# Kernel tuning notes

Measured on AMD Instinct MI355X. Metric: run time of the kernel, lower is better.

Reference implementation:

```python
import jax, jax.numpy as jnp
import numpy as np
import math

N = 50000        # nodes
DEG = 16         # regular out-degree -> E = N*DEG edges, grouped by source node
B = 64           # graphs in batch
F = 128          # num_node_features
H = 128          # nhid == enhid
RATIO = 0.5      # edge_ratio
NUM_CONVS = 3
E = N * DEG


def setup_inputs() -> dict:
    key = jax.random.key(0)
    ks = jax.random.split(key, 18)
    s = 0.05
    x = jax.random.normal(ks[0], (N, F), jnp.float32)
    edge_src = jnp.repeat(jnp.arange(N, dtype=jnp.int32), DEG)          # sorted by src
    edge_dst = jax.random.randint(ks[1], (E,), 0, N, jnp.int32)
    batch = ((jnp.arange(N) * B) // N).astype(jnp.int32)                 # sorted graph ids
    edge_attr = jnp.ones((E, 1), jnp.float32)                            # edge_attr=None branch
    inp = {"x": x, "edge_attr": edge_attr, "edge_src": edge_src,
           "edge_dst": edge_dst, "batch": batch}
    # GCNConv weights: [F->H, H->H, H->H]
    inp["W_gcn0"] = jax.random.normal(ks[2], (F, H), jnp.float32) * s
    inp["b_gcn0"] = jnp.zeros((H,), jnp.float32)
    inp["W_gcn1"] = jax.random.normal(ks[3], (H, H), jnp.float32) * s
    inp["b_gcn1"] = jnp.zeros((H,), jnp.float32)
    inp["W_gcn2"] = jax.random.normal(ks[4], (H, H), jnp.float32) * s
    inp["b_gcn2"] = jnp.zeros((H,), jnp.float32)
    # EGNN edge convs: [1->H, H->H]
    inp["W_eg0"] = jax.random.normal(ks[5], (1, H), jnp.float32) * s
    inp["b_eg0"] = jnp.zeros((H,), jnp.float32)
    inp["W_eg1"] = jax.random.normal(ks[6], (H, H), jnp.float32) * s
    inp["b_eg1"] = jnp.zeros((H,), jnp.float32)
    # score convs: [H->1, H->1]
    inp["W_sc0"] = jax.random.normal(ks[7], (H, 1), jnp.float32) * s
    inp["b_sc0"] = jnp.zeros((1,), jnp.float32)
    inp["W_sc1"] = jax.random.normal(ks[8], (H, 1), jnp.float32) * s
    inp["b_sc1"] = jnp.zeros((1,), jnp.float32)
    return inp


def _gcn(x, src, dst, ew, W, b):
    # PyG GCNConv: add self-loops (weight 1), symmetric deg normalization, aggregate at dst.
    n = x.shape[0]
    loop = jnp.arange(n, dtype=src.dtype)
    src2 = jnp.concatenate([src, loop])
    dst2 = jnp.concatenate([dst, loop])
    ew2 = jnp.concatenate([ew, jnp.ones((n,), ew.dtype)])
    deg = jax.ops.segment_sum(ew2, dst2, n)
    dinv = jnp.where(deg > 0, jax.lax.rsqrt(jnp.maximum(deg, 1e-12)), 0.0)
    norm = dinv[src2] * dinv[dst2] * ew2                                  # [E+n]
    msg = (x @ W)[src2] * norm[:, None]                                    # gather + scale
    return jax.ops.segment_sum(msg, dst2, n) + b                           # scatter-add


def _egnn(e, src, W, b):
    # Edge conv: scatter edge features to their source node, gather back, linear map.
    agg = jax.ops.segment_sum(e, src, N)
    return agg[src] @ W + b


def _pool(h, batch):
    gmax = jax.ops.segment_max(h, batch, B)
    gsum = jax.ops.segment_sum(h, batch, B)
    cnt = jax.ops.segment_sum(jnp.ones((h.shape[0],), h.dtype), batch, B)
    gmean = gsum / cnt[:, None]
    return jnp.concatenate([gmax, gmean, gsum], axis=1)                    # [B, 3H]


def reference(x, edge_attr, edge_src, edge_dst, batch,
              W_gcn0, b_gcn0, W_gcn1, b_gcn1, W_gcn2, b_gcn2,
              W_eg0, b_eg0, W_eg1, b_eg1, W_sc0, b_sc0, W_sc1, b_sc1):
    gW = [W_gcn0, W_gcn1, W_gcn2]
    gb = [b_gcn0, b_gcn1, b_gcn2]
    eW = [W_eg0, W_eg1]
    eb = [b_eg0, b_eg1]
    sW = [W_sc0, W_sc1]
    sb = [b_sc0, b_sc1]
    src, dst = edge_src, edge_dst
    deg = DEG
    ew = jnp.ones((src.shape[0],), jnp.float32)
    h = x
    ea = edge_attr
    xs = jnp.zeros((B, 3 * H), jnp.float32)
    for i in range(NUM_CONVS):
        h = jax.nn.relu(_gcn(h, src, dst, ew, gW[i], gb[i]))
        if i < NUM_CONVS - 1:
            ea = jax.nn.relu(_egnn(ea, src, eW[i], eb[i]))
            score = jnp.tanh(_egnn(ea, src, sW[i], sb[i])[:, 0])           # [E_cur]
            k = math.ceil(RATIO * deg)                                      # per-src-node top-k
            vals, idx = jax.lax.top_k(score.reshape(N, deg), k)             # [N,k]
            dst = jnp.take_along_axis(dst.reshape(N, deg), idx, axis=1).reshape(-1)
            flat = (jnp.arange(N)[:, None] * deg + idx).reshape(-1)
            ea = ea[flat]
            src = jnp.repeat(jnp.arange(N, dtype=src.dtype), k)
            ew = jnp.clip(vals.reshape(-1), 0.0, 1.0)
            deg = k
        xs = xs + _pool(h, batch)
    return xs
```

## Files before the change

### kernel.cpp

```cpp
#include <hip/hip_runtime.h>
#include <math.h>

#define NNODES 50000
#define DEGREE 16
#define NGRAPH 64
#define CAP 64
#define LDA 136
#define NXCD 8
#define XRANGE (NNODES / NXCD)
#define NTILE 782
#define ACHUNK 784
#define BCAP 192

typedef unsigned short u16;
typedef unsigned int u32;
typedef unsigned long long u64;
using short8 = __attribute__((ext_vector_type(8))) short;
using f32x4  = __attribute__((ext_vector_type(4))) float;
using fv4    = __attribute__((ext_vector_type(4))) float;
using u16x4  = __attribute__((ext_vector_type(4))) unsigned short;

__device__ __forceinline__ u16 f2bf(float f) {
  union { float f; u32 u; } v; v.f = f;
  u32 u = v.u;
  return (u16)((u + 0x7FFFu + ((u >> 16) & 1u)) >> 16);
}
__device__ __forceinline__ float2 bf2x2(u32 u) {
  union { u32 u; float f; } lo, hi;
  lo.u = (u & 0xFFFFu) << 16; hi.u = u & 0xFFFF0000u;
  return make_float2(lo.f, hi.f);
}
__device__ __forceinline__ u32 pack2(float x, float y) {
  return (u32)f2bf(x) | ((u32)f2bf(y) << 16);
}
__device__ __forceinline__ int lowerb(const int* b, int n, int v) {
  int lo = 0, hi = n;
  while (lo < hi) { int m = (lo + hi) >> 1; if (b[m] < v) lo = m + 1; else hi = m; }
  return lo;
}

__global__ __launch_bounds__(256) void k_init(
    const float* __restrict__ eattr, const float* __restrict__ x,
    const float* __restrict__ weg, const float* __restrict__ beg,
    const float* __restrict__ wsc, const float* __restrict__ bsc,
    const float* __restrict__ W0, const float* __restrict__ W1,
    const float* __restrict__ W2, const float* __restrict__ W3,
    float* __restrict__ ew1, float* __restrict__ agg0,
    u16* __restrict__ xb, u16* __restrict__ Wt,
    const int* __restrict__ edst, int* __restrict__ cnt,
    int* __restrict__ slots, int2* __restrict__ stag, int* __restrict__ scnt) {
  __shared__ int2 lbuf[NXCD * BCAP];
  __shared__ int lcnt[NXCD];
  int b = blockIdx.x, t = threadIdx.x;
  if (b < 6250) {
    int i = b * 256 + t;
    fv4 v = __builtin_nontemporal_load(&reinterpret_cast<const fv4*>(x)[i]);
    u16x4 o = {f2bf(v.x), f2bf(v.y), f2bf(v.z), f2bf(v.w)};
    reinterpret_cast<u16x4*>(xb)[i] = o;
    if (i < NNODES) {
      const fv4* p = reinterpret_cast<const fv4*>(eattr + (size_t)i * DEGREE);
      float s = 0.f;
#pragma unroll
      for (int j = 0; j < 4; ++j) {
        fv4 w = __builtin_nontemporal_load(&p[j]);
        s += w.x + w.y + w.z + w.w;
      }
      agg0[i] = s;
      float sc = 0.f;
      for (int k = 0; k < 128; ++k) {
        float e = fmaxf(fmaf(s, weg[k], beg[k]), 0.f);
        sc = fmaf(e, wsc[k], sc);
      }
      float v1 = tanhf(fmaf(16.f, sc, bsc[0]));
      ew1[i] = fminf(fmaxf(v1, 0.f), 1.f);
    }
  } else if (b < 6506) {
    int idx = (b - 6250) * 256 + t;
    int which = idx >> 14, r = idx & 16383;
    int k = r >> 7, n = r & 127;
    const float* W = which == 0 ? W0 : which == 1 ? W1 : which == 2 ? W2 : W3;
    Wt[which * 16384 + n * 128 + k] = f2bf(W[k * 128 + n]);
  } else {
    int b2 = b - 6506;
    if (t < NXCD) lcnt[t] = 0;
    __syncthreads();
    int e0 = b2 * ACHUNK;
    for (int k = 0; k < ACHUNK; k += 256) {
      int idx = k + t;
      int e = e0 + idx;
      if (idx < ACHUNK && e < NNODES * DEGREE) {
        int d = edst[e];
        u32 r = (u32)d / (u32)XRANGE;
        int pos = atomicAdd(&lcnt[r], 1);
        if (pos < BCAP) {
          lbuf[r * BCAP + pos] = make_int2(e, d);
        } else {
          int gp = atomicAdd(&cnt[d], 1);
          if (gp < CAP) slots[(size_t)d * CAP + gp] = e;
        }
      }
    }
    __syncthreads();
    for (int idx = t; idx < NXCD * BCAP; idx += 256) {
      int r = idx / BCAP, i = idx - r * BCAP;
      if (i < min(lcnt[r], BCAP))
        stag[((size_t)r * 1024 + b2) * BCAP + i] = lbuf[idx];
    }
    if (t < NXCD) scnt[t * 1024 + b2] = min(lcnt[t], BCAP);
  }
}

__global__ __launch_bounds__(256) void k_fillB(
    const int2* __restrict__ stag, const int* __restrict__ scnt,
    int* __restrict__ cnt, int* __restrict__ slots) {
  int kk = blockIdx.x;
  int r = kk & (NXCD - 1), sub = kk >> 3;
  for (int q = 0; q < 8; ++q) {
    int sb = sub * 8 + q;
    int c = scnt[r * 1024 + sb];
    const int2* src = &stag[((size_t)r * 1024 + sb) * BCAP];
    for (int i = threadIdx.x; i < c; i += 256) {
      int2 v = src[i];
      int pos = atomicAdd(&cnt[v.y], 1);
      if (pos < CAP) slots[(size_t)v.y * CAP + pos] = v.x;
    }
  }
}

__global__ __launch_bounds__(256) void k_gemmF(
    int nGemm, const u16* __restrict__ A, const u16* __restrict__ WtA,
    u16* __restrict__ outA,
    int nEg, const float* __restrict__ agg0, const float* __restrict__ weg,
    const float* __restrict__ beg, const u16* __restrict__ WtE,
    const float* __restrict__ beE, const float* __restrict__ wsc1,
    const float* __restrict__ bs1, float* __restrict__ ewOut) {
  __shared__ u16 Bs[128 * LDA];
  __shared__ u16 As[64 * LDA];
  int b = blockIdx.x, t = threadIdx.x;
  int eg = (b >= nGemm);
  const u16* Wsrc = eg ? WtE : WtA;
  for (int i = t; i < 2048; i += 256) {
    int r = i >> 4, c = (i & 15) << 3;
    *reinterpret_cast<uint4*>(&Bs[r * LDA + c]) =
        *reinterpret_cast<const uint4*>(&Wsrc[r * 128 + c]);
  }
  int m0 = (eg ? (b - nGemm) : b) * 64;
  if (eg) {
    for (int idx = t; idx < 64 * 128; idx += 256) {
      int r = idx >> 7, k = idx & 127;
      int row = m0 + r;
      float a = (row < NNODES) ? agg0[row] : 0.f;
      float v = 8.f * fmaxf(fmaf(a, weg[k], beg[k]), 0.f);
      As[r * LDA + k] = f2bf(v);
    }
  } else {
    for (int i = t; i < 1024; i += 256) {
      int r = i >> 4, c = (i & 15) << 3;
      int row = m0 + r;
      uint4 v = make_uint4(0u, 0u, 0u, 0u);
      if (row < NNODES) v = *reinterpret_cast<const uint4*>(&A[(size_t)row * 128 + c]);
      *reinterpret_cast<uint4*>(&As[r * LDA + c]) = v;
    }
  }
  __syncthreads();
  int wave = t >> 6, lane = t & 63;
  int lm = lane & 15, quad = lane >> 4;
  f32x4 z = {0.f, 0.f, 0.f, 0.f};
  f32x4 acc[8];
#pragma unroll
  for (int n = 0; n < 8; ++n) acc[n] = z;
  const u16* arow = &As[(wave * 16 + lm) * LDA + quad * 8];
#pragma unroll
  for (int kc = 0; kc < 4; ++kc) {
    short8 af = *reinterpret_cast<const short8*>(arow + kc * 32);
#pragma unroll
    for (int n = 0; n < 8; ++n) {
      short8 bf = *reinterpret_cast<const short8*>(
          &Bs[(n * 16 + lm) * LDA + kc * 32 + quad * 8]);
      acc[n] = __builtin_amdgcn_mfma_f32_16x16x32_bf16(af, bf, acc[n], 0, 0, 0);
    }
  }
  if (!eg) {
#pragma unroll
    for (int n = 0; n < 8; ++n) {
      int col = n * 16 + lm;
#pragma unroll
      for (int r = 0; r < 4; ++r) {
        int row = m0 + wave * 16 + quad * 4 + r;
        if (row < NNODES) outA[(size_t)row * 128 + col] = f2bf(acc[n][r]);
      }
    }
  } else {
    float s0 = 0.f, s1 = 0.f, s2 = 0.f, s3 = 0.f;
#pragma unroll
    for (int n = 0; n < 8; ++n) {
      int col = n * 16 + lm;
      float bb = beE[col], wv = wsc1[col];
      s0 = fmaf(fmaxf(acc[n][0] + bb, 0.f), wv, s0);
      s1 = fmaf(fmaxf(acc[n][1] + bb, 0.f), wv, s1);
      s2 = fmaf(fmaxf(acc[n][2] + bb, 0.f), wv, s2);
      s3 = fmaf(fmaxf(acc[n][3] + bb, 0.f), wv, s3);
    }
#pragma unroll
    for (int m = 8; m >= 1; m >>= 1) {
      s0 += __shfl_xor(s0, m, 64);
      s1 += __shfl_xor(s1, m, 64);
      s2 += __shfl_xor(s2, m, 64);
      s3 += __shfl_xor(s3, m, 64);
    }
    if (lm == 0) {
      float bsv = bs1[0];
      float sv[4] = {s0, s1, s2, s3};
#pragma unroll
      for (int r = 0; r < 4; ++r) {
        int row = m0 + wave * 16 + quad * 4 + r;
        if (row < NNODES) {
          float v = tanhf(fmaf(8.f, sv[r], bsv));
          ewOut[row] = fminf(fmaxf(v, 0.f), 1.f);
        }
      }
    }
  }
}

__global__ __launch_bounds__(256) void k_dinv2(
    const int* __restrict__ cnt, const int* __restrict__ slots,
    const float* __restrict__ ew1, float* __restrict__ dinv1,
    float* __restrict__ wsrc1,
    const float* __restrict__ ew2, float* __restrict__ dinv2,
    float* __restrict__ wsrc2) {
  int n = (int)((blockIdx.x * blockDim.x + threadIdx.x) >> 6);
  int lane = threadIdx.x & 63;
  if (n >= NNODES) return;
  int c = min(cnt[n], CAP);
  u32 ent = 0;
  if (lane < c) ent = (u32)slots[(size_t)n * CAP + lane];
  u32 j = ent & 15u;
  int src = (int)(ent >> 4);
  float e1 = 0.f, e2 = 0.f;
  if (lane < c && j < 8u) {
    e1 = ew1[src];
    if (j < 4u) e2 = ew2[src];
  }
#pragma unroll
  for (int m = 32; m >= 1; m >>= 1) {
    e1 += __shfl_xor(e1, m, 64);
    e2 += __shfl_xor(e2, m, 64);
  }
  float d1 = rsqrtf(1.0f + e1);
  float d2 = rsqrtf(1.0f + e2);
  if (lane == 0) {
    dinv1[n] = d1; wsrc1[n] = d1 * ew1[n];
    dinv2[n] = d2; wsrc2[n] = d2 * ew2[n];
  }
}

__global__ __launch_bounds__(256) void k_aggp(
    int nAgg, const u16* __restrict__ xwb, const int* __restrict__ cnt,
    const int* __restrict__ slots, const float* __restrict__ wsrc,
    const float* __restrict__ dinv, const float* __restrict__ bias,
    u16* __restrict__ hout, int keep, int l0mode,
    const u16* __restrict__ hpool, const int* __restrict__ batch,
    float* __restrict__ out, int poolAdd) {
  __shared__ float P[16 * 64];
  int b = blockIdx.x, t = threadIdx.x;
  int lane = t & 63;
  if (b < nAgg) {
    int n = (b * 256 + t) >> 6;
    if (n >= NNODES) return;
    int c = min(cnt[n], CAP);
    u32 e = 0;
    if (lane < c) e = (u32)slots[(size_t)n * CAP + lane];
    int kc; u32 ce;
    if (keep < 16) {
      bool valid = (lane < c) && ((e & 15u) < (u32)keep);
      u64 mask = __ballot(valid);
      kc = (int)__popcll(mask);
      u64 lt = ((u64)1 << lane) - 1;
      int pos = valid ? (int)__popcll(mask & lt) : 63 - (int)__popcll((~mask) & lt);
      ce = (u32)__builtin_amdgcn_ds_permute(pos << 2, (int)e);
    } else { kc = c; ce = e; }
    int sl = 0; float wl = 0.f;
    if (lane < kc) {
      sl = (int)(ce >> 4);
      wl = l0mode ? rsqrtf(1.0f + (float)min(cnt[sl], CAP)) : wsrc[sl];
    }
    const u32* base = reinterpret_cast<const u32*>(xwb);
    float2 acc = make_float2(0.f, 0.f);
    int i = 0;
    for (; i + 8 <= kc; i += 8) {
      u32 r[8]; float w[8];
#pragma unroll
      for (int j = 0; j < 8; ++j) {
        int s = __shfl(sl, i + j, 64);
        w[j] = __shfl(wl, i + j, 64);
        r[j] = base[(size_t)s * 64 + lane];
      }
#pragma unroll
      for (int j = 0; j < 8; ++j) {
        float2 v = bf2x2(r[j]);
        acc.x = fmaf(w[j], v.x, acc.x);
        acc.y = fmaf(w[j], v.y, acc.y);
      }
    }
    for (; i + 4 <= kc; i += 4) {
      u32 r[4]; float w[4];
#pragma unroll
      for (int j = 0; j < 4; ++j) {
        int s = __shfl(sl, i + j, 64);
        w[j] = __shfl(wl, i + j, 64);
        r[j] = base[(size_t)s * 64 + lane];
      }
#pragma unroll
      for (int j = 0; j < 4; ++j) {
        float2 v = bf2x2(r[j]);
        acc.x = fmaf(w[j], v.x, acc.x);
        acc.y = fmaf(w[j], v.y, acc.y);
      }
    }
    for (; i < kc; ++i) {
      int s = __shfl(sl, i, 64);
      float w = __shfl(wl, i, 64);
      float2 v = bf2x2(base[(size_t)s * 64 + lane]);
      acc.x = fmaf(w, v.x, acc.x);
      acc.y = fmaf(w, v.y, acc.y);
    }
    float di = l0mode ? rsqrtf(1.0f + (float)c) : dinv[n];
    float2 self = bf2x2(base[(size_t)n * 64 + lane]);
    float2 bv = reinterpret_cast<const float2*>(bias)[lane];
    float rx = fmaxf(fmaf(di, acc.x, fmaf(di * di, self.x, bv.x)), 0.f);
    float ry = fmaxf(fmaf(di, acc.y, fmaf(di * di, self.y, bv.y)), 0.f);
    reinterpret_cast<u32*>(hout + (size_t)n * 128)[lane] = pack2(rx, ry);
  } else {
    int g = b - nAgg;
    int rg = t >> 6;
    int lo = lowerb(batch, NNODES, g);
    int hi = lowerb(batch, NNODES, g + 1);
    const u32* hb = reinterpret_cast<const u32*>(hpool);
    float mxx = 0.f, mxy = 0.f, smx = 0.f, smy = 0.f;
    int n = lo + rg;
    for (; n + 28 < hi; n += 32) {
      u32 r[8];
#pragma unroll
      for (int jj = 0; jj < 8; ++jj) r[jj] = hb[(size_t)(n + 4 * jj) * 64 + lane];
#pragma unroll
      for (int jj = 0; jj < 8; ++jj) {
        float2 v = bf2x2(r[jj]);
        mxx = fmaxf(mxx, v.x); mxy = fmaxf(mxy, v.y);
        smx += v.x; smy += v.y;
      }
    }
    for (; n < hi; n += 4) {
      float2 v = bf2x2(hb[(size_t)n * 64 + lane]);
      mxx = fmaxf(mxx, v.x); mxy = fmaxf(mxy, v.y);
      smx += v.x; smy += v.y;
    }
    P[(rg * 4 + 0) * 64 + lane] = mxx;
    P[(rg * 4 + 1) * 64 + lane] = mxy;
    P[(rg * 4 + 2) * 64 + lane] = smx;
    P[(rg * 4 + 3) * 64 + lane] = smy;
    __syncthreads();
    if (t < 64) {
      float amx = 0.f, amy = 0.f, asx = 0.f, asy = 0.f;
#pragma unroll
      for (int rgi = 0; rgi < 4; ++rgi) {
        amx = fmaxf(amx, P[(rgi * 4 + 0) * 64 + t]);
        amy = fmaxf(amy, P[(rgi * 4 + 1) * 64 + t]);
        asx += P[(rgi * 4 + 2) * 64 + t];
        asy += P[(rgi * 4 + 3) * 64 + t];
      }
      float cf = (float)(hi - lo);
      int f0 = 2 * t;
      float* og = out + g * 384;
      if (poolAdd) {
        og[f0] += amx;             og[f0 + 1] += amy;
        og[128 + f0] += asx / cf;  og[128 + f0 + 1] += asy / cf;
        og[256 + f0] += asx;       og[256 + f0 + 1] += asy;
      } else {
        og[f0] = amx;              og[f0 + 1] = amy;
        og[128 + f0] = asx / cf;   og[128 + f0 + 1] = asy / cf;
        og[256 + f0] = asx;        og[256 + f0 + 1] = asy;
      }
    }
  }
}

extern "C" void kernel_launch(void* const* d_in, const int* in_sizes, int n_in,
                              void* d_out, int out_size, void* d_ws, size_t ws_size,
                              hipStream_t stream) {
  const float* x     = (const float*)d_in[0];
  const float* eattr = (const float*)d_in[1];
  const int*   edst  = (const int*)d_in[3];
  const int*   batch = (const int*)d_in[4];
  const float* Wg0 = (const float*)d_in[5];  const float* bg0 = (const float*)d_in[6];
  const float* Wg1 = (const float*)d_in[7];  const float* bg1 = (const float*)d_in[8];
  const float* Wg2 = (const float*)d_in[9];  const float* bg2 = (const float*)d_in[10];
  const float* We0 = (const float*)d_in[11]; const float* be0 = (const float*)d_in[12];
  const float* We1 = (const float*)d_in[13]; const float* be1 = (const float*)d_in[14];
  const float* Ws0 = (const float*)d_in[15]; const float* bs0 = (const float*)d_in[16];
  const float* Ws1 = (const float*)d_in[17]; const float* bs1 = (const float*)d_in[18];
  float* out = (float*)d_out;

  char* ws = (char*)d_ws;
  const size_t NBH = (size_t)NNODES * 128 * 2;
  size_t off = 0;
  auto alloc = [&](size_t bytes) { void* p = ws + off; off = (off + bytes + 255) & ~(size_t)255; return p; };
  u16*   Xb    = (u16*)alloc(NBH);
  u16*   XWb   = (u16*)alloc(NBH);
  u16*   Hb0   = (u16*)alloc(NBH);
  u16*   Hb1   = (u16*)alloc(NBH);
  u16*   Hb2   = (u16*)alloc(NBH);
  u16*   Wtb   = (u16*)alloc(4 * 128 * 128 * 2);
  int*   slots = (int*)alloc((size_t)NNODES * CAP * 4);
  int*   cnt   = (int*)alloc((size_t)NNODES * 4);
  int2*  stag  = (int2*)alloc((size_t)NXCD * 1024 * BCAP * 8);
  int*   scnt  = (int*)alloc((size_t)NXCD * 1024 * 4);
  float* agg0  = (float*)alloc((size_t)NNODES * 4);
  float* ew1   = (float*)alloc((size_t)NNODES * 4);
  float* ew2   = (float*)alloc((size_t)NNODES * 4);
  float* dinv1 = (float*)alloc((size_t)NNODES * 4);
  float* wsrc1 = (float*)alloc((size_t)NNODES * 4);
  float* dinv2 = (float*)alloc((size_t)NNODES * 4);
  float* wsrc2 = (float*)alloc((size_t)NNODES * 4);

  hipMemsetAsync(cnt, 0, (size_t)NNODES * 4, stream);
  k_init<<<7530, 256, 0, stream>>>(eattr, x, We0, be0, Ws0, bs0,
                                   Wg0, Wg1, Wg2, We1, ew1, agg0, Xb, Wtb,
                                   edst, cnt, slots, stag, scnt);
  k_fillB<<<1024, 256, 0, stream>>>(stag, scnt, cnt, slots);
  k_gemmF<<<2 * NTILE, 256, 0, stream>>>(
      NTILE, Xb, Wtb, XWb,
      NTILE, agg0, We0, be0, Wtb + 3 * 16384, be1, Ws1, bs1, ew2);
  k_aggp<<<12500, 256, 0, stream>>>(12500, XWb, cnt, slots, nullptr, nullptr, bg0,
                                    Hb0, 16, 1, nullptr, batch, nullptr, 0);
  k_dinv2<<<12500, 256, 0, stream>>>(cnt, slots, ew1, dinv1, wsrc1,
                                     ew2, dinv2, wsrc2);
  k_gemmF<<<NTILE, 256, 0, stream>>>(
      NTILE, Hb0, Wtb + 16384, XWb,
      0, nullptr, nullptr, nullptr, nullptr, nullptr, nullptr, nullptr, nullptr);
  k_aggp<<<12500 + NGRAPH, 256, 0, stream>>>(12500, XWb, cnt, slots, wsrc1, dinv1,
                                             bg1, Hb1, 8, 0, Hb0, batch, out, 0);
  k_gemmF<<<NTILE, 256, 0, stream>>>(
      NTILE, Hb1, Wtb + 2 * 16384, XWb,
      0, nullptr, nullptr, nullptr, nullptr, nullptr, nullptr, nullptr, nullptr);
  k_aggp<<<12500 + NGRAPH, 256, 0, stream>>>(12500, XWb, cnt, slots, wsrc2, dinv2,
                                             bg2, Hb2, 4, 0, Hb1, batch, out, 1);
  k_aggp<<<NGRAPH, 256, 0, stream>>>(0, nullptr, cnt, slots, nullptr, nullptr,
                                     nullptr, nullptr, 0, 0, Hb2, batch, out, 1);
}
```

Baseline: 338.7 us.

## Fuse dinv kernel into first aggregation and vectorize gathers to 16-byte rows

Removes the separate k_dinv2 launch by computing the layer-1/2 degree normalizers inside the layer-0 aggregation pass, which already loads the same slot lists. The gather is restructured so each wave reads four neighbor rows at a time with 16-byte loads per lane (16 lanes per row), then reduces across quarter-waves with shuffles. The pooling path is likewise switched to uint4 loads with a new LDS reduction layout. This trades wider, fewer memory transactions for extra shuffle reductions and padded work when the neighbor count is not a multiple of 4.

```diff
diff --git a/kernel.cpp b/kernel.cpp
--- a/kernel.cpp
+++ b/kernel.cpp
@@ -37,6 +37,25 @@
   int lo = 0, hi = n;
   while (lo < hi) { int m = (lo + hi) >> 1; if (b[m] < v) lo = m + 1; else hi = m; }
   return lo;
+}
+
+__device__ __forceinline__ void cons8(uint4 v, float w, float* acc) {
+  float2 p;
+  p = bf2x2(v.x); acc[0] = fmaf(w, p.x, acc[0]); acc[1] = fmaf(w, p.y, acc[1]);
+  p = bf2x2(v.y); acc[2] = fmaf(w, p.x, acc[2]); acc[3] = fmaf(w, p.y, acc[3]);
+  p = bf2x2(v.z); acc[4] = fmaf(w, p.x, acc[4]); acc[5] = fmaf(w, p.y, acc[5]);
+  p = bf2x2(v.w); acc[6] = fmaf(w, p.x, acc[6]); acc[7] = fmaf(w, p.y, acc[7]);
+}
+__device__ __forceinline__ void consP(uint4 v, float* mx, float* sm) {
+  float2 p;
+  p = bf2x2(v.x);
+  mx[0] = fmaxf(mx[0], p.x); sm[0] += p.x; mx[1] = fmaxf(mx[1], p.y); sm[1] += p.y;
+  p = bf2x2(v.y);
+  mx[2] = fmaxf(mx[2], p.x); sm[2] += p.x; mx[3] = fmaxf(mx[3], p.y); sm[3] += p.y;
+  p = bf2x2(v.z);
+  mx[4] = fmaxf(mx[4], p.x); sm[4] += p.x; mx[5] = fmaxf(mx[5], p.y); sm[5] += p.y;
+  p = bf2x2(v.w);
+  mx[6] = fmaxf(mx[6], p.x); sm[6] += p.x; mx[7] = fmaxf(mx[7], p.y); sm[7] += p.y;
 }
 
 __global__ __launch_bounds__(256) void k_init(
@@ -223,54 +242,45 @@
   }
 }
 
-__global__ __launch_bounds__(256) void k_dinv2(
-    const int* __restrict__ cnt, const int* __restrict__ slots,
-    const float* __restrict__ ew1, float* __restrict__ dinv1,
-    float* __restrict__ wsrc1,
-    const float* __restrict__ ew2, float* __restrict__ dinv2,
-    float* __restrict__ wsrc2) {
-  int n = (int)((blockIdx.x * blockDim.x + threadIdx.x) >> 6);
-  int lane = threadIdx.x & 63;
-  if (n >= NNODES) return;
-  int c = min(cnt[n], CAP);
-  u32 ent = 0;
-  if (lane < c) ent = (u32)slots[(size_t)n * CAP + lane];
-  u32 j = ent & 15u;
-  int src = (int)(ent >> 4);
-  float e1 = 0.f, e2 = 0.f;
-  if (lane < c && j < 8u) {
-    e1 = ew1[src];
-    if (j < 4u) e2 = ew2[src];
-  }
-#pragma unroll
-  for (int m = 32; m >= 1; m >>= 1) {
-    e1 += __shfl_xor(e1, m, 64);
-    e2 += __shfl_xor(e2, m, 64);
-  }
-  float d1 = rsqrtf(1.0f + e1);
-  float d2 = rsqrtf(1.0f + e2);
-  if (lane == 0) {
-    dinv1[n] = d1; wsrc1[n] = d1 * ew1[n];
-    dinv2[n] = d2; wsrc2[n] = d2 * ew2[n];
-  }
-}
-
 __global__ __launch_bounds__(256) void k_aggp(
     int nAgg, const u16* __restrict__ xwb, const int* __restrict__ cnt,
     const int* __restrict__ slots, const float* __restrict__ wsrc,
     const float* __restrict__ dinv, const float* __restrict__ bias,
     u16* __restrict__ hout, int keep, int l0mode,
     const u16* __restrict__ hpool, const int* __restrict__ batch,
-    float* __restrict__ out, int poolAdd) {
-  __shared__ float P[16 * 64];
+    float* __restrict__ out, int poolAdd,
+    const float* __restrict__ ew1g, float* __restrict__ dv1,
+    float* __restrict__ ws1,
+    const float* __restrict__ ew2g, float* __restrict__ dv2,
+    float* __restrict__ ws2) {
+  __shared__ float P[1024];
   int b = blockIdx.x, t = threadIdx.x;
   int lane = t & 63;
+  int q = lane >> 4, li = lane & 15;
   if (b < nAgg) {
     int n = (b * 256 + t) >> 6;
     if (n >= NNODES) return;
     int c = min(cnt[n], CAP);
     u32 e = 0;
     if (lane < c) e = (u32)slots[(size_t)n * CAP + lane];
+    if (l0mode) {
+      u32 j = e & 15u; int srcn = (int)(e >> 4);
+      float e1 = 0.f, e2 = 0.f;
+      if (lane < c && j < 8u) {
+        e1 = ew1g[srcn];
+        if (j < 4u) e2 = ew2g[srcn];
+      }
+#pragma unroll
+      for (int m = 32; m >= 1; m >>= 1) {
+        e1 += __shfl_xor(e1, m, 64);
+        e2 += __shfl_xor(e2, m, 64);
+      }
+      if (lane == 0) {
+        float d1 = rsqrtf(1.0f + e1), d2 = rsqrtf(1.0f + e2);
+        dv1[n] = d1; ws1[n] = d1 * ew1g[n];
+        dv2[n] = d2; ws2[n] = d2 * ew2g[n];
+      }
+    }
     int kc; u32 ce;
     if (keep < 16) {
       bool valid = (lane < c) && ((e & 15u) < (u32)keep);
@@ -285,101 +295,103 @@
       sl = (int)(ce >> 4);
       wl = l0mode ? rsqrtf(1.0f + (float)min(cnt[sl], CAP)) : wsrc[sl];
     }
-    const u32* base = reinterpret_cast<const u32*>(xwb);
-    float2 acc = make_float2(0.f, 0.f);
-    int i = 0;
-    for (; i + 8 <= kc; i += 8) {
-      u32 r[8]; float w[8];
-#pragma unroll
-      for (int j = 0; j < 8; ++j) {
-        int s = __shfl(sl, i + j, 64);
-        w[j] = __shfl(wl, i + j, 64);
-        r[j] = base[(size_t)s * 64 + lane];
-      }
-#pragma unroll
-      for (int j = 0; j < 8; ++j) {
-        float2 v = bf2x2(r[j]);
-        acc.x = fmaf(w[j], v.x, acc.x);
-        acc.y = fmaf(w[j], v.y, acc.y);
-      }
-    }
-    for (; i + 4 <= kc; i += 4) {
-      u32 r[4]; float w[4];
-#pragma unroll
-      for (int j = 0; j < 4; ++j) {
-        int s = __shfl(sl, i + j, 64);
-        w[j] = __shfl(wl, i + j, 64);
-        r[j] = base[(size_t)s * 64 + lane];
-      }
-#pragma unroll
-      for (int j = 0; j < 4; ++j) {
-        float2 v = bf2x2(r[j]);
-        acc.x = fmaf(w[j], v.x, acc.x);
-        acc.y = fmaf(w[j], v.y, acc.y);
-      }
-    }
-    for (; i < kc; ++i) {
-      int s = __shfl(sl, i, 64);
-      float w = __shfl(wl, i, 64);
-      float2 v = bf2x2(base[(size_t)s * 64 + lane]);
-      acc.x = fmaf(w, v.x, acc.x);
-      acc.y = fmaf(w, v.y, acc.y);
+    const uint4* b4 = reinterpret_cast<const uint4*>(xwb);
+    uint4 selfv = b4[n * 16 + li];
+    float acc[8] = {0.f, 0.f, 0.f, 0.f, 0.f, 0.f, 0.f, 0.f};
+    for (int i = 0; i < kc; i += 16) {
+      int r0 = i + q, r1 = i + 4 + q, r2 = i + 8 + q, r3 = i + 12 + q;
+      int s0 = __shfl(sl, r0, 64); float w0 = __shfl(wl, r0, 64);
+      int s1 = __shfl(sl, r1, 64); float w1 = __shfl(wl, r1, 64);
+      int s2 = __shfl(sl, r2, 64); float w2 = __shfl(wl, r2, 64);
+      int s3 = __shfl(sl, r3, 64); float w3 = __shfl(wl, r3, 64);
+      if (r0 >= kc) { s0 = n; w0 = 0.f; }
+      if (r1 >= kc) { s1 = n; w1 = 0.f; }
+      if (r2 >= kc) { s2 = n; w2 = 0.f; }
+      if (r3 >= kc) { s3 = n; w3 = 0.f; }
+      uint4 v0 = b4[s0 * 16 + li];
+      uint4 v1 = selfv, v2 = selfv, v3 = selfv;
+      if (i + 4 < kc)  v1 = b4[s1 * 16 + li];
+      if (i + 8 < kc)  v2 = b4[s2 * 16 + li];
+      if (i + 12 < kc) v3 = b4[s3 * 16 + li];
+      cons8(v0, w0, acc);
+      cons8(v1, w1, acc);
+      cons8(v2, w2, acc);
+      cons8(v3, w3, acc);
+    }
+#pragma unroll
+    for (int k = 0; k < 8; ++k) {
+      acc[k] += __shfl_xor(acc[k], 16, 64);
+      acc[k] += __shfl_xor(acc[k], 32, 64);
     }
     float di = l0mode ? rsqrtf(1.0f + (float)c) : dinv[n];
-    float2 self = bf2x2(base[(size_t)n * 64 + lane]);
-    float2 bv = reinterpret_cast<const float2*>(bias)[lane];
-    float rx = fmaxf(fmaf(di, acc.x, fmaf(di * di, self.x, bv.x)), 0.f);
-    float ry = fmaxf(fmaf(di, acc.y, fmaf(di * di, self.y, bv.y)), 0.f);
-    reinterpret_cast<u32*>(hout + (size_t)n * 128)[lane] = pack2(rx, ry);
+    float dd = di * di;
+    const f32x4* bp = reinterpret_cast<const f32x4*>(bias);
+    f32x4 bv0 = bp[li * 2], bv1 = bp[li * 2 + 1];
+    float2 p0 = bf2x2(selfv.x), p1 = bf2x2(selfv.y),
+           p2 = bf2x2(selfv.z), p3 = bf2x2(selfv.w);
+    float r0 = fmaxf(fmaf(di, acc[0], fmaf(dd, p0.x, bv0.x)), 0.f);
+    float r1 = fmaxf(fmaf(di, acc[1], fmaf(dd, p0.y, bv0.y)), 0.f);
+    float r2 = fmaxf(fmaf(di, acc[2], fmaf(dd, p1.x, bv0.z)), 0.f);
+    float r3 = fmaxf(fmaf(di, acc[3], fmaf(dd, p1.y, bv0.w)), 0.f);
+    float r4 = fmaxf(fmaf(di, acc[4], fmaf(dd, p2.x, bv1.x)), 0.f);
+    float r5 = fmaxf(fmaf(di, acc[5], fmaf(dd, p2.y, bv1.y)), 0.f);
+    float r6 = fmaxf(fmaf(di, acc[6], fmaf(dd, p3.x, bv1.z)), 0.f);
+    float r7 = fmaxf(fmaf(di, acc[7], fmaf(dd, p3.y, bv1.w)), 0.f);
+    if (q == 0) {
+      uint4 o;
+      o.x = pack2(r0, r1); o.y = pack2(r2, r3);
+      o.z = pack2(r4, r5); o.w = pack2(r6, r7);
+      reinterpret_cast<uint4*>(hout + (size_t)n * 128)[li] = o;
+    }
   } else {
     int g = b - nAgg;
-    int rg = t >> 6;
+    int wv = t >> 6;
     int lo = lowerb(batch, NNODES, g);
     int hi = lowerb(batch, NNODES, g + 1);
-    const u32* hb = reinterpret_cast<const u32*>(hpool);
-    float mxx = 0.f, mxy = 0.f, smx = 0.f, smy = 0.f;
-    int n = lo + rg;
-    for (; n + 28 < hi; n += 32) {
-      u32 r[8];
-#pragma unroll
-      for (int jj = 0; jj < 8; ++jj) r[jj] = hb[(size_t)(n + 4 * jj) * 64 + lane];
-#pragma unroll
-      for (int jj = 0; jj < 8; ++jj) {
-        float2 v = bf2x2(r[jj]);
-        mxx = fmaxf(mxx, v.x); mxy = fmaxf(mxy, v.y);
-        smx += v.x; smy += v.y;
-      }
-    }
-    for (; n < hi; n += 4) {
-      float2 v = bf2x2(hb[(size_t)n * 64 + lane]);
-      mxx = fmaxf(mxx, v.x); mxy = fmaxf(mxy, v.y);
-      smx += v.x; smy += v.y;
-    }
-    P[(rg * 4 + 0) * 64 + lane] = mxx;
-    P[(rg * 4 + 1) * 64 + lane] = mxy;
-    P[(rg * 4 + 2) * 64 + lane] = smx;
-    P[(rg * 4 + 3) * 64 + lane] = smy;
+    const uint4* hb4 = reinterpret_cast<const uint4*>(hpool);
+    float mx[8] = {0.f, 0.f, 0.f, 0.f, 0.f, 0.f, 0.f, 0.f};
+    float sm[8] = {0.f, 0.f, 0.f, 0.f, 0.f, 0.f, 0.f, 0.f};
+    int n = lo + wv * 4 + q;
+    for (; n + 48 < hi; n += 64) {
+      uint4 v0 = hb4[(size_t)n * 16 + li];
+      uint4 v1 = hb4[(size_t)(n + 16) * 16 + li];
+      uint4 v2 = hb4[(size_t)(n + 32) * 16 + li];
+      uint4 v3 = hb4[(size_t)(n + 48) * 16 + li];
+      consP(v0, mx, sm); consP(v1, mx, sm);
+      consP(v2, mx, sm); consP(v3, mx, sm);
+    }
+    for (; n < hi; n += 16) {
+      uint4 v = hb4[(size_t)n * 16 + li];
+      consP(v, mx, sm);
+    }
+#pragma unroll
+    for (int k = 0; k < 8; ++k) {
+      mx[k] = fmaxf(mx[k], __shfl_xor(mx[k], 16, 64));
+      mx[k] = fmaxf(mx[k], __shfl_xor(mx[k], 32, 64));
+      sm[k] += __shfl_xor(sm[k], 16, 64);
+      sm[k] += __shfl_xor(sm[k], 32, 64);
+    }
+    if (q == 0) {
+#pragma unroll
+      for (int k = 0; k < 8; ++k) {
+        P[(wv * 16 + li) * 16 + k] = mx[k];
+        P[(wv * 16 + li) * 16 + 8 + k] = sm[k];
+      }
+    }
     __syncthreads();
-    if (t < 64) {
-      float amx = 0.f, amy = 0.f, asx = 0.f, asy = 0.f;
-#pragma unroll
-      for (int rgi = 0; rgi < 4; ++rgi) {
-        amx = fmaxf(amx, P[(rgi * 4 + 0) * 64 + t]);
-        amy = fmaxf(amy, P[(rgi * 4 + 1) * 64 + t]);
-        asx += P[(rgi * 4 + 2) * 64 + t];
-        asy += P[(rgi * 4 + 3) * 64 + t];
-      }
+    if (t < 128) {
+      int li2 = t >> 3, k = t & 7;
+      int o0 = li2 * 16 + k, o1 = o0 + 8;
+      float m = fmaxf(fmaxf(P[o0], P[256 + o0]),
+                      fmaxf(P[512 + o0], P[768 + o0]));
+      float s = P[o1] + P[256 + o1] + P[512 + o1] + P[768 + o1];
       float cf = (float)(hi - lo);
-      int f0 = 2 * t;
+      int col = li2 * 8 + k;
       float* og = out + g * 384;
       if (poolAdd) {
-        og[f0] += amx;             og[f0 + 1] += amy;
-        og[128 + f0] += asx / cf;  og[128 + f0 + 1] += asy / cf;
-        og[256 + f0] += asx;       og[256 + f0 + 1] += asy;
+        og[col] += m; og[128 + col] += s / cf; og[256 + col] += s;
       } else {
-        og[f0] = amx;              og[f0 + 1] = amy;
-        og[128 + f0] = asx / cf;   og[128 + f0 + 1] = asy / cf;
-        og[256 + f0] = asx;        og[256 + f0 + 1] = asy;
+        og[col] = m;  og[128 + col] = s / cf;  og[256 + col] = s;
       }
     }
   }
@@ -432,19 +444,24 @@
       NTILE, Xb, Wtb, XWb,
       NTILE, agg0, We0, be0, Wtb + 3 * 16384, be1, Ws1, bs1, ew2);
   k_aggp<<<12500, 256, 0, stream>>>(12500, XWb, cnt, slots, nullptr, nullptr, bg0,
-                                    Hb0, 16, 1, nullptr, batch, nullptr, 0);
-  k_dinv2<<<12500, 256, 0, stream>>>(cnt, slots, ew1, dinv1, wsrc1,
-                                     ew2, dinv2, wsrc2);
+                                    Hb0, 16, 1, nullptr, batch, nullptr, 0,
+                                    ew1, dinv1, wsrc1, ew2, dinv2, wsrc2);
   k_gemmF<<<NTILE, 256, 0, stream>>>(
       NTILE, Hb0, Wtb + 16384, XWb,
       0, nullptr, nullptr, nullptr, nullptr, nullptr, nullptr, nullptr, nullptr);
   k_aggp<<<12500 + NGRAPH, 256, 0, stream>>>(12500, XWb, cnt, slots, wsrc1, dinv1,
-                                             bg1, Hb1, 8, 0, Hb0, batch, out, 0);
+                                             bg1, Hb1, 8, 0, Hb0, batch, out, 0,
+                                             nullptr, nullptr, nullptr,
+                                             nullptr, nullptr, nullptr);
   k_gemmF<<<NTILE, 256, 0, stream>>>(
       NTILE, Hb1, Wtb + 2 * 16384, XWb,
       0, nullptr, nullptr, nullptr, nullptr, nullptr, nullptr, nullptr, nullptr);
   k_aggp<<<12500 + NGRAPH, 256, 0, stream>>>(12500, XWb, cnt, slots, wsrc2, dinv2,
-                                             bg2, Hb2, 4, 0, Hb1, batch, out, 1);
+                                             bg2, Hb2, 4, 0, Hb1, batch, out, 1,
+                                             nullptr, nullptr, nullptr,
+                                             nullptr, nullptr, nullptr);
   k_aggp<<<NGRAPH, 256, 0, stream>>>(0, nullptr, cnt, slots, nullptr, nullptr,
-                                     nullptr, nullptr, 0, 0, Hb2, batch, out, 1);
-}
+                                     nullptr, nullptr, 0, 0, Hb2, batch, out, 1,
+                                     nullptr, nullptr, nullptr,
+                                     nullptr, nullptr, nullptr);
+}
```

New measurement: 327.9 us. 3.2% less time.
